# Performance work log

Hardware: AMD Instinct MI355X
Metric: run time of the kernel (lower is better)

The kernel has to match this reference:

```python
import jax, jax.numpy as jnp
import numpy as np

NORM_EPS = 1e-6


def setup_inputs() -> dict:
    key = jax.random.key(0)
    k1, k2 = jax.random.split(key)
    in_features, out_features = 4096, 4096
    x = jax.random.normal(k1, (2, 2048, in_features), dtype=jnp.float32)
    scale = 1.0 / np.sqrt(in_features)
    weight = jax.random.normal(k2, (out_features, in_features), dtype=jnp.float32) * scale
    norm_weight = jnp.ones((in_features,), dtype=jnp.float32)
    return {"x": x, "weight": weight, "norm_weight": norm_weight}


def reference(x, weight, norm_weight):
    # RMSNorm over the last dim
    rms = jnp.sqrt(jnp.mean(x * x, axis=-1, keepdims=True) + NORM_EPS)
    x_n = x / rms * norm_weight
    # ternary weight quantization (absmean scale alpha)
    alpha = jnp.maximum(jnp.mean(jnp.abs(weight)), 1e-10)
    w_q = jnp.clip(jnp.round(weight / alpha), -1.0, 1.0)
    # per-token int8 activation quantization (absmax scale gamma)
    gamma = jnp.maximum(jnp.max(jnp.abs(x_n), axis=-1, keepdims=True), 1e-10)
    x_q = jnp.clip(jnp.round(x_n * 127.0 / gamma), -128.0, 127.0)
    # rescaled matmul: y = x_q @ w_q.T * (alpha * gamma / 127)
    y = jnp.einsum('bsk,nk->bsn', x_q, w_q) * (alpha * gamma / 127.0)
    return y
```

## Files before the change

### kernel.cpp

```cpp
#include <hip/hip_runtime.h>
#include <cstdint>
#include <cstddef>


#define KD 4096
#define MD 4096
#define ND 4096

#define WBLK 512

typedef int i32x4 __attribute__((ext_vector_type(4)));

__device__ __forceinline__ void gl2lds16(const signed char* g, signed char* l) {
  __builtin_amdgcn_global_load_lds(
      (const __attribute__((address_space(1))) void*)g,
      (__attribute__((address_space(3))) void*)l, 16, 0, 0);
}

__device__ __forceinline__ float wave_sum(float v) {
#pragma unroll
  for (int off = 32; off; off >>= 1) v += __shfl_down(v, off, 64);
  return v;
}
__device__ __forceinline__ float wave_max(float v) {
#pragma unroll
  for (int off = 32; off; off >>= 1) v = fmaxf(v, __shfl_down(v, off, 64));
  return v;
}


__global__ __launch_bounds__(256) void k_alpha_part(const float* __restrict__ w,
                                                    float* __restrict__ part) {
  __shared__ float red[4];
  const int tid = threadIdx.x;
  const float4* w4 = (const float4*)(w + (size_t)blockIdx.x * 4096);
  float s = 0.f;
#pragma unroll
  for (int i = 0; i < 4; ++i) {
    float4 v = w4[i * 256 + tid];
    s += fabsf(v.x) + fabsf(v.y) + fabsf(v.z) + fabsf(v.w);
  }
  s = wave_sum(s);
  if ((tid & 63) == 0) red[tid >> 6] = s;
  __syncthreads();
  if (tid == 0) part[blockIdx.x] = (red[0] + red[1]) + (red[2] + red[3]);
}


__device__ __forceinline__ uint32_t qw4(float4 v, float alpha) {
  int q0 = (int)fminf(fmaxf(rintf(v.x / alpha), -1.f), 1.f);
  int q1 = (int)fminf(fmaxf(rintf(v.y / alpha), -1.f), 1.f);
  int q2 = (int)fminf(fmaxf(rintf(v.z / alpha), -1.f), 1.f);
  int q3 = (int)fminf(fmaxf(rintf(v.w / alpha), -1.f), 1.f);
  return (uint32_t)(q0 & 255) | ((uint32_t)(q1 & 255) << 8) |
         ((uint32_t)(q2 & 255) << 16) | ((uint32_t)(q3 & 255) << 24);
}

__global__ __launch_bounds__(256) void k_quant_all(const float* __restrict__ w,
                                                   const float* __restrict__ x,
                                                   const float* __restrict__ nw,
                                                   const float* __restrict__ part,
                                                   signed char* __restrict__ wq,
                                                   signed char* __restrict__ xq,
                                                   float* __restrict__ gamma,
                                                   float* __restrict__ alpha_out) {
  const int tid = threadIdx.x;
  const int bid = blockIdx.x;
  __shared__ float red[4];
  __shared__ float red2[4];

  if (bid < 4096) {
    const int row = bid;
    const float4* x4 = (const float4*)(x + (size_t)row * 4096);
    const float4* n4 = (const float4*)nw;
    float4 xv[4], nv[4];
#pragma unroll
    for (int i = 0; i < 4; ++i) {
      xv[i] = x4[i * 256 + tid];
      nv[i] = n4[i * 256 + tid];
    }
    float ss = 0.f, mx = 0.f;
#pragma unroll
    for (int i = 0; i < 4; ++i) {
      ss += xv[i].x * xv[i].x + xv[i].y * xv[i].y + xv[i].z * xv[i].z +
            xv[i].w * xv[i].w;
      mx = fmaxf(mx,
                 fmaxf(fmaxf(fabsf(xv[i].x * nv[i].x), fabsf(xv[i].y * nv[i].y)),
                       fmaxf(fabsf(xv[i].z * nv[i].z), fabsf(xv[i].w * nv[i].w))));
    }
    ss = wave_sum(ss);
    mx = wave_max(mx);
    if ((tid & 63) == 0) {
      red[tid >> 6] = ss;
      red2[tid >> 6] = mx;
    }
    __syncthreads();
    const float tot = (red[0] + red[1]) + (red[2] + red[3]);
    const float rms = sqrtf(tot * (1.0f / 4096.0f) + 1e-6f);
    const float mxr = fmaxf(fmaxf(red2[0], red2[1]), fmaxf(red2[2], red2[3]));
    const float g = fmaxf(mxr / rms, 1e-10f);
    if (tid == 0) gamma[row] = g;
    const float inv = 127.0f / (rms * g);

    uint32_t* xqi = (uint32_t*)(xq + (size_t)row * 4096);
#pragma unroll
    for (int i = 0; i < 4; ++i) {
      const int f = i * 256 + tid;
      int q0 = (int)fminf(fmaxf(rintf(xv[i].x * nv[i].x * inv), -128.f), 127.f);
      int q1 = (int)fminf(fmaxf(rintf(xv[i].y * nv[i].y * inv), -128.f), 127.f);
      int q2 = (int)fminf(fmaxf(rintf(xv[i].z * nv[i].z * inv), -128.f), 127.f);
      int q3 = (int)fminf(fmaxf(rintf(xv[i].w * nv[i].w * inv), -128.f), 127.f);
      xqi[f] = (uint32_t)(q0 & 255) | ((uint32_t)(q1 & 255) << 8) |
               ((uint32_t)(q2 & 255) << 16) | ((uint32_t)(q3 & 255) << 24);
    }
  } else {
    const int wb = bid - 4096;
    float s = 0.f;
#pragma unroll
    for (int i = 0; i < 16; ++i) s += part[i * 256 + tid];
    s = wave_sum(s);
    if ((tid & 63) == 0) red[tid >> 6] = s;
    __syncthreads();
    const float alpha =
        fmaxf(((red[0] + red[1]) + (red[2] + red[3])) * (1.0f / 16777216.0f),
              1e-10f);
    if (wb == 0 && tid == 0) alpha_out[0] = alpha;

    const float4* w4 = (const float4*)w;
    uint32_t* wqi = (uint32_t*)wq;
#pragma unroll 1
    for (int k = 0; k < 32; k += 4) {
      const int f0 = (wb * 32 + k) * 256 + tid;
      float4 v0 = w4[f0];
      float4 v1 = w4[f0 + 256];
      float4 v2 = w4[f0 + 512];
      float4 v3 = w4[f0 + 768];
      wqi[f0] = qw4(v0, alpha);
      wqi[f0 + 256] = qw4(v1, alpha);
      wqi[f0 + 512] = qw4(v2, alpha);
      wqi[f0 + 768] = qw4(v3, alpha);
    }
  }
}


#define BM 256
#define BN 256
#define BK 64

__global__ __launch_bounds__(512, 2) void k_gemm(const signed char* __restrict__ xq,
                                                 const signed char* __restrict__ wq,
                                                 const float* __restrict__ gamma,
                                                 const float* __restrict__ alpha_p,
                                                 float* __restrict__ out) {
  __shared__ __align__(16) signed char LDS_[65536];
  const int tid = threadIdx.x;
  const int lane = tid & 63;
  const int wave = tid >> 6;
  const int wm = (wave >> 2) * 128;
  const int wn = (wave & 3) * 64;
  const int quad = lane >> 4;
  const int l16 = lane & 15;

  const int x = blockIdx.x & 7;
  const int r = blockIdx.x >> 3;
  const int bm = ((x & 3) * 4 + (r >> 3)) * BM;
  const int bn = ((x >> 2) * 8 + (r & 7)) * BN;

  const int lr = lane >> 2;
  const int sc = (lane & 3) ^ ((lane >> 3) & 3);
  const int rb0 = wave * 16;
  const int rb1 = (8 + wave) * 16;
  const signed char* ag0 = xq + (size_t)(bm + rb0 + lr) * KD + sc * 16;
  const signed char* ag1 = xq + (size_t)(bm + rb1 + lr) * KD + sc * 16;
  const signed char* bg0 = wq + (size_t)(bn + rb0 + lr) * KD + sc * 16;
  const signed char* bg1 = wq + (size_t)(bn + rb1 + lr) * KD + sc * 16;
  const int lA0 = rb0 * BK;
  const int lA1 = rb1 * BK;

  const int pos = (quad ^ ((l16 >> 1) & 3)) * 16;

  i32x4 acc[8][4];
#pragma unroll
  for (int i = 0; i < 8; ++i)
#pragma unroll
    for (int j = 0; j < 4; ++j) acc[i][j] = (i32x4){0, 0, 0, 0};

  gl2lds16(ag0, LDS_ + lA0);
  gl2lds16(ag1, LDS_ + lA1);
  gl2lds16(bg0, LDS_ + 16384 + lA0);
  gl2lds16(bg1, LDS_ + 16384 + lA1);
  __syncthreads();

  for (int t = 0; t < 64; ++t) {
    const int c = t & 1;
    const signed char* Ab = LDS_ + c * 32768;
    const signed char* Bb = Ab + 16384;
    signed char* An = LDS_ + (c ^ 1) * 32768;
    signed char* Bn = An + 16384;
    const size_t kn = (size_t)(t + 1) * BK;
    const bool more = (t < 63);

    i32x4 bf[4], af[2];

#pragma unroll
    for (int p = 0; p < 4; ++p) {
      if (p == 0) {
#pragma unroll
        for (int ni = 0; ni < 4; ++ni)
          bf[ni] = *(const i32x4*)&Bb[(wn + ni * 16 + l16) * BK + pos];
      }
#pragma unroll
      for (int j = 0; j < 2; ++j)
        af[j] = *(const i32x4*)&Ab[(wm + (p * 2 + j) * 16 + l16) * BK + pos];

      if (more) {
        if (p == 0) {
          gl2lds16(ag0 + kn, An + lA0);
          gl2lds16(ag1 + kn, An + lA1);
        } else if (p == 1) {
          gl2lds16(bg0 + kn, Bn + lA0);
          gl2lds16(bg1 + kn, Bn + lA1);
        }
      }
      __builtin_amdgcn_s_setprio(1);
#pragma unroll
      for (int j = 0; j < 2; ++j)
#pragma unroll
        for (int ni = 0; ni < 4; ++ni)
          acc[p * 2 + j][ni] = __builtin_amdgcn_mfma_i32_16x16x64_i8(
              af[j], bf[ni], acc[p * 2 + j][ni], 0, 0, 0);
      __builtin_amdgcn_s_setprio(0);
    }
    __syncthreads();
  }

  const float alpha = alpha_p[0];
#pragma unroll
  for (int mi = 0; mi < 8; ++mi) {
#pragma unroll
    for (int r2 = 0; r2 < 4; ++r2) {
      const int m = bm + wm + mi * 16 + quad * 4 + r2;
      const float s = (alpha * gamma[m]) / 127.0f;
#pragma unroll
      for (int ni = 0; ni < 4; ++ni) {
        const int n = bn + wn + ni * 16 + l16;
        out[(size_t)m * ND + n] = (float)acc[mi][ni][r2] * s;
      }
    }
  }
}


extern "C" void kernel_launch(void* const* d_in, const int* in_sizes, int n_in,
                              void* d_out, int out_size, void* d_ws, size_t ws_size,
                              hipStream_t stream) {
  const float* x = (const float*)d_in[0];
  const float* w = (const float*)d_in[1];
  const float* nw = (const float*)d_in[2];
  float* out = (float*)d_out;

  char* ws = (char*)d_ws;
  signed char* xq = (signed char*)ws;
  signed char* wq = (signed char*)(ws + ((size_t)1 << 24));
  float* gamma = (float*)(ws + ((size_t)2 << 24));
  float* part = (float*)(ws + ((size_t)2 << 24) + 16384);
  float* alpha = (float*)(ws + ((size_t)2 << 24) + 32768);

  k_alpha_part<<<4096, 256, 0, stream>>>(w, part);
  k_quant_all<<<4096 + WBLK, 256, 0, stream>>>(w, x, nw, part, wq, xq, gamma, alpha);
  k_gemm<<<dim3(256), dim3(512), 0, stream>>>(xq, wq, gamma, alpha, out);
}
```

Before: 232.4 us.

## Load weight fragments directly to registers, bypassing LDS, and add intra-tile barriers

Weight (B) fragments are no longer staged through LDS. Each lane loads its own 16-byte slices straight from global memory into registers and double-buffers them across K steps. This halves LDS usage, which may allow higher occupancy, and removes the B LDS reads. Each wave now issues uncoalesced per-lane global loads that duplicate reads across the two M-waves sharing a column. Extra s_barrier calls are added around each MFMA phase to keep waves in lockstep, which adds synchronization cost.

```diff
diff --git a/kernel.cpp b/kernel.cpp
--- a/kernel.cpp
+++ b/kernel.cpp
@@ -153,7 +153,7 @@
                                                  const float* __restrict__ gamma,
                                                  const float* __restrict__ alpha_p,
                                                  float* __restrict__ out) {
-  __shared__ __align__(16) signed char LDS_[65536];
+  __shared__ __align__(16) signed char As_[2 * 16384];
   const int tid = threadIdx.x;
   const int lane = tid & 63;
   const int wave = tid >> 6;
@@ -173,56 +173,51 @@
   const int rb1 = (8 + wave) * 16;
   const signed char* ag0 = xq + (size_t)(bm + rb0 + lr) * KD + sc * 16;
   const signed char* ag1 = xq + (size_t)(bm + rb1 + lr) * KD + sc * 16;
-  const signed char* bg0 = wq + (size_t)(bn + rb0 + lr) * KD + sc * 16;
-  const signed char* bg1 = wq + (size_t)(bn + rb1 + lr) * KD + sc * 16;
   const int lA0 = rb0 * BK;
   const int lA1 = rb1 * BK;
 
   const int pos = (quad ^ ((l16 >> 1) & 3)) * 16;
 
+  const signed char* bgf[4];
+#pragma unroll
+  for (int ni = 0; ni < 4; ++ni)
+    bgf[ni] = wq + (size_t)(bn + wn + ni * 16 + l16) * KD + quad * 16;
+
   i32x4 acc[8][4];
 #pragma unroll
   for (int i = 0; i < 8; ++i)
 #pragma unroll
     for (int j = 0; j < 4; ++j) acc[i][j] = (i32x4){0, 0, 0, 0};
 
-  gl2lds16(ag0, LDS_ + lA0);
-  gl2lds16(ag1, LDS_ + lA1);
-  gl2lds16(bg0, LDS_ + 16384 + lA0);
-  gl2lds16(bg1, LDS_ + 16384 + lA1);
+  i32x4 bf[4], bfn[4], af[2];
+
+  gl2lds16(ag0, As_ + lA0);
+  gl2lds16(ag1, As_ + lA1);
+#pragma unroll
+  for (int ni = 0; ni < 4; ++ni) bf[ni] = *(const i32x4*)bgf[ni];
   __syncthreads();
 
   for (int t = 0; t < 64; ++t) {
     const int c = t & 1;
-    const signed char* Ab = LDS_ + c * 32768;
-    const signed char* Bb = Ab + 16384;
-    signed char* An = LDS_ + (c ^ 1) * 32768;
-    signed char* Bn = An + 16384;
+    const signed char* Ab = As_ + c * 16384;
+    signed char* An = As_ + (c ^ 1) * 16384;
     const size_t kn = (size_t)(t + 1) * BK;
     const bool more = (t < 63);
 
-    i32x4 bf[4], af[2];
-
 #pragma unroll
     for (int p = 0; p < 4; ++p) {
-      if (p == 0) {
-#pragma unroll
-        for (int ni = 0; ni < 4; ++ni)
-          bf[ni] = *(const i32x4*)&Bb[(wn + ni * 16 + l16) * BK + pos];
-      }
 #pragma unroll
       for (int j = 0; j < 2; ++j)
         af[j] = *(const i32x4*)&Ab[(wm + (p * 2 + j) * 16 + l16) * BK + pos];
 
-      if (more) {
-        if (p == 0) {
-          gl2lds16(ag0 + kn, An + lA0);
-          gl2lds16(ag1 + kn, An + lA1);
-        } else if (p == 1) {
-          gl2lds16(bg0 + kn, Bn + lA0);
-          gl2lds16(bg1 + kn, Bn + lA1);
-        }
+      if (more && p == 0) {
+#pragma unroll
+        for (int ni = 0; ni < 4; ++ni)
+          bfn[ni] = *(const i32x4*)(bgf[ni] + kn);
+        gl2lds16(ag0 + kn, An + lA0);
+        gl2lds16(ag1 + kn, An + lA1);
       }
+      __builtin_amdgcn_s_barrier();
       __builtin_amdgcn_s_setprio(1);
 #pragma unroll
       for (int j = 0; j < 2; ++j)
@@ -231,8 +226,13 @@
           acc[p * 2 + j][ni] = __builtin_amdgcn_mfma_i32_16x16x64_i8(
               af[j], bf[ni], acc[p * 2 + j][ni], 0, 0, 0);
       __builtin_amdgcn_s_setprio(0);
+      if (p < 3) __builtin_amdgcn_s_barrier();
     }
     __syncthreads();
+    if (more) {
+#pragma unroll
+      for (int ni = 0; ni < 4; ++ni) bf[ni] = bfn[ni];
+    }
   }
 
   const float alpha = alpha_p[0];
```

Result: slower. 262.5 us (+13.0%).

## Triple-buffer LDS tiles with prefetch distance two and explicit vmcnt waits

Applied to the files above, without the earlier changes.

Grows the int8 GEMM's shared-memory staging from two to three 32 KB buffers, so global-to-LDS loads run two K-steps ahead. The end-of-iteration __syncthreads is replaced by an s_waitcnt vmcnt(4) plus a raw barrier, which waits only on the tile needed next. It also adds barriers between the MFMA phases inside each K-step to keep waves in lockstep. The aim is to hide more global-load latency. The cost is 96 KB of LDS per block, which may stop two 512-thread blocks from sharing a CU as the launch bounds request, and the extra barriers add synchronisation overhead.

```diff
diff --git a/kernel.cpp b/kernel.cpp
--- a/kernel.cpp
+++ b/kernel.cpp
@@ -153,7 +153,7 @@
                                                  const float* __restrict__ gamma,
                                                  const float* __restrict__ alpha_p,
                                                  float* __restrict__ out) {
-  __shared__ __align__(16) signed char LDS_[65536];
+  __shared__ __align__(16) signed char As_[3 * 32768];
   const int tid = threadIdx.x;
   const int lane = tid & 63;
   const int wave = tid >> 6;
@@ -186,20 +186,26 @@
 #pragma unroll
     for (int j = 0; j < 4; ++j) acc[i][j] = (i32x4){0, 0, 0, 0};
 
-  gl2lds16(ag0, LDS_ + lA0);
-  gl2lds16(ag1, LDS_ + lA1);
-  gl2lds16(bg0, LDS_ + 16384 + lA0);
-  gl2lds16(bg1, LDS_ + 16384 + lA1);
-  __syncthreads();
-
+  gl2lds16(ag0, As_ + lA0);
+  gl2lds16(ag1, As_ + lA1);
+  gl2lds16(bg0, As_ + 16384 + lA0);
+  gl2lds16(bg1, As_ + 16384 + lA1);
+  gl2lds16(ag0 + BK, As_ + 32768 + lA0);
+  gl2lds16(ag1 + BK, As_ + 32768 + lA1);
+  gl2lds16(bg0 + BK, As_ + 32768 + 16384 + lA0);
+  gl2lds16(bg1 + BK, As_ + 32768 + 16384 + lA1);
+  asm volatile("s_waitcnt vmcnt(4)" ::: "memory");
+  __builtin_amdgcn_s_barrier();
+
+  int cb = 0;
   for (int t = 0; t < 64; ++t) {
-    const int c = t & 1;
-    const signed char* Ab = LDS_ + c * 32768;
+    const signed char* Ab = As_ + cb * 32768;
     const signed char* Bb = Ab + 16384;
-    signed char* An = LDS_ + (c ^ 1) * 32768;
+    const int sb = (cb == 0) ? 2 : cb - 1;
+    signed char* An = As_ + sb * 32768;
     signed char* Bn = An + 16384;
-    const size_t kn = (size_t)(t + 1) * BK;
-    const bool more = (t < 63);
+    const size_t kn = (size_t)(t + 2) * BK;
+    const bool st = (t < 62);
 
     i32x4 bf[4], af[2];
 
@@ -214,7 +220,7 @@
       for (int j = 0; j < 2; ++j)
         af[j] = *(const i32x4*)&Ab[(wm + (p * 2 + j) * 16 + l16) * BK + pos];
 
-      if (more) {
+      if (st) {
         if (p == 0) {
           gl2lds16(ag0 + kn, An + lA0);
           gl2lds16(ag1 + kn, An + lA1);
@@ -223,6 +229,7 @@
           gl2lds16(bg1 + kn, Bn + lA1);
         }
       }
+      __builtin_amdgcn_s_barrier();
       __builtin_amdgcn_s_setprio(1);
 #pragma unroll
       for (int j = 0; j < 2; ++j)
@@ -231,8 +238,17 @@
           acc[p * 2 + j][ni] = __builtin_amdgcn_mfma_i32_16x16x64_i8(
               af[j], bf[ni], acc[p * 2 + j][ni], 0, 0, 0);
       __builtin_amdgcn_s_setprio(0);
-    }
-    __syncthreads();
+      if (p < 3) __builtin_amdgcn_s_barrier();
+    }
+
+    if (t < 62) {
+      asm volatile("s_waitcnt vmcnt(4)" ::: "memory");
+      __builtin_amdgcn_s_barrier();
+    } else if (t == 62) {
+      asm volatile("s_waitcnt vmcnt(0)" ::: "memory");
+      __builtin_amdgcn_s_barrier();
+    }
+    cb = (cb == 2) ? 0 : cb + 1;
   }
 
   const float alpha = alpha_p[0];
```

New measurement: 231.7 us. About the same (-0.3%).
